# Kernel optimization log

Hardware: AMD Instinct MI355X
Metric: run time of the kernel (lower is better)

The kernel has to match this reference:

```python
import jax, jax.numpy as jnp
import numpy as np

# static config (levels=4, CDA=False branch -> self_attn_4, scale=4, f=False)
SHAPES = [(80, 80), (40, 40), (20, 20), (10, 10)]
D = 256; NH = 8; NL = 4; NP = 4; DFF = 1024; DH = D // NH
L = sum(h * w for h, w in SHAPES)  # 8500
B = 1


def layer_norm(x, g, b, eps=1e-5):
    m = jnp.mean(x, axis=-1, keepdims=True)
    v = jnp.mean((x - m) ** 2, axis=-1, keepdims=True)
    return (x - m) * jax.lax.rsqrt(v + eps) * g + b


def ms_deform_attn_core(value, loc, attn):
    # value: [B, L, NH, DH]; loc: [B, Lq, NH, NL, NP, 2] in [0,1]; attn: [B, Lq, NH, NL, NP]
    Bq, Lq = loc.shape[0], loc.shape[1]
    out = jnp.zeros((Bq, NH, Lq, DH), value.dtype)
    start = 0
    for lvl, (Hl, Wl) in enumerate(SHAPES):
        v = value[:, start:start + Hl * Wl]          # [B, HW, NH, DH]
        start += Hl * Wl
        v = v.transpose(0, 2, 1, 3)                  # [B, NH, HW, DH]
        ll = loc[:, :, :, lvl]                       # [B, Lq, NH, NP, 2]
        # grid_sample semantics: align_corners=False, padding_mode='zeros'
        x = ll[..., 0] * Wl - 0.5
        y = ll[..., 1] * Hl - 0.5
        x0 = jnp.floor(x); y0 = jnp.floor(y)
        acc = jnp.zeros((Bq, NH, Lq, NP, DH), value.dtype)
        for dy in (0, 1):
            for dx in (0, 1):
                xi = x0 + dx; yi = y0 + dy
                w = (1.0 - jnp.abs(x - xi)) * (1.0 - jnp.abs(y - yi))  # [B,Lq,NH,NP]
                valid = (xi >= 0) & (xi < Wl) & (yi >= 0) & (yi < Hl)
                xi_c = jnp.clip(xi, 0, Wl - 1).astype(jnp.int32)
                yi_c = jnp.clip(yi, 0, Hl - 1).astype(jnp.int32)
                lin = (yi_c * Wl + xi_c).transpose(0, 2, 1, 3).reshape(Bq, NH, Lq * NP)
                g = jnp.take_along_axis(v, lin[..., None], axis=2).reshape(Bq, NH, Lq, NP, DH)
                wv = (w * valid.astype(w.dtype)).transpose(0, 2, 1, 3)[..., None]
                acc = acc + g * wv
        aw = attn[:, :, :, lvl].transpose(0, 2, 1, 3)[..., None]  # [B,NH,Lq,NP,1]
        out = out + jnp.sum(acc * aw, axis=3)
    return out.transpose(0, 2, 1, 3).reshape(Bq, Lq, NH * DH)


def setup_inputs():
    key = jax.random.key(0)
    ks = jax.random.split(key, 24)
    s = 0.02
    d = {}
    d['src'] = jax.random.normal(ks[0], (B, L, D), jnp.float32)
    d['pos'] = jax.random.normal(ks[1], (B, L, D), jnp.float32)
    d['reference_points'] = jax.random.uniform(ks[2], (B, L, NL, 2), jnp.float32)
    d['spatial_shapes'] = jnp.array(SHAPES, jnp.int32)
    d['level_start_index'] = jnp.array(np.cumsum([0] + [h * w for h, w in SHAPES[:-1]]), jnp.int32)
    d['scale'] = 4
    # MSDeformAttn params
    d['Wo'] = jax.random.normal(ks[3], (D, NH * NL * NP * 2), jnp.float32) * s
    d['bo'] = jax.random.normal(ks[4], (NH * NL * NP * 2,), jnp.float32) * s
    d['Wa'] = jax.random.normal(ks[5], (D, NH * NL * NP), jnp.float32) * s
    d['ba'] = jax.random.normal(ks[6], (NH * NL * NP,), jnp.float32) * s
    d['Wv'] = jax.random.normal(ks[7], (D, D), jnp.float32) * s
    d['bv'] = jnp.zeros((D,), jnp.float32)
    d['Wout'] = jax.random.normal(ks[8], (D, D), jnp.float32) * s
    d['bout'] = jnp.zeros((D,), jnp.float32)
    # FFN + LayerNorms
    d['W1'] = jax.random.normal(ks[9], (D, DFF), jnp.float32) * s
    d['b1'] = jnp.zeros((DFF,), jnp.float32)
    d['W2'] = jax.random.normal(ks[10], (DFF, D), jnp.float32) * s
    d['b2'] = jnp.zeros((D,), jnp.float32)
    d['g1'] = jnp.ones((D,), jnp.float32); d['be1'] = jnp.zeros((D,), jnp.float32)
    d['g2'] = jnp.ones((D,), jnp.float32); d['be2'] = jnp.zeros((D,), jnp.float32)
    return d


def reference(src, pos, reference_points, spatial_shapes, level_start_index, scale,
              Wo, bo, Wa, ba, Wv, bv, Wout, bout, W1, b1, W2, b2, g1, be1, g2, be2):
    Bq, Lq, _ = src.shape
    q = src + pos  # with_pos_embed
    # sampling offsets & attention weights (softmax over levels*points)
    off = (q @ Wo + bo).reshape(Bq, Lq, NH, NL, NP, 2)
    attn = jax.nn.softmax((q @ Wa + ba).reshape(Bq, Lq, NH, NL * NP), axis=-1)
    attn = attn.reshape(Bq, Lq, NH, NL, NP)
    value = (src @ Wv + bv).reshape(Bq, L, NH, DH)
    # offset normalizer is (W, H) per level
    normalizer = jnp.stack([spatial_shapes[:, 1], spatial_shapes[:, 0]], -1).astype(src.dtype)
    loc = reference_points[:, :, None, :, None, :] + off / normalizer[None, None, None, :, None, :]
    src2 = ms_deform_attn_core(value, loc, attn) @ Wout + bout
    # residual + norm1 (dropout = eval identity)
    x = layer_norm(src + src2, g1, be1)
    # FFN
    ffn = jax.nn.relu(x @ W1 + b1) @ W2 + b2
    x = layer_norm(x + ffn, g2, be2)
    return x
```

## Files before the change

kernel.cpp:

```cpp
#include <hip/hip_runtime.h>
#include <hip/hip_bf16.h>
#include <string.h>

#define D 256
#define NH 8
#define DH 32
#define NL 4
#define NP 4
#define DFF 1024
#define LTOT 8500

typedef __bf16 bf16x8 __attribute__((ext_vector_type(8)));
typedef float floatx4 __attribute__((ext_vector_type(4)));

__device__ inline unsigned bpack(float a, float b) {
    __hip_bfloat16 ha = __float2bfloat16(a), hb = __float2bfloat16(b);
    unsigned short ua, ub;
    memcpy(&ua, &ha, 2); memcpy(&ub, &hb, 2);
    return (unsigned)ua | ((unsigned)ub << 16);
}

__device__ inline void gload16(const void* g, void* l) {
    __builtin_amdgcn_global_load_lds((const __attribute__((address_space(1))) void*)g,
                                     (__attribute__((address_space(3))) void*)l,
                                     16, 0, 0);
}

__global__ void transpose_all(const float* W0, const float* W1_, const float* W2_,
                              const float* W3, const float* W4, const float* W5,
                              __hip_bfloat16* T0, __hip_bfloat16* T1, __hip_bfloat16* T2,
                              __hip_bfloat16* T3, __hip_bfloat16* T4, __hip_bfloat16* T5,
                              const float* src, const float* pos,
                              __hip_bfloat16* qb, __hip_bfloat16* srcb) {
    int id = blockIdx.x;
    if (id >= 736) {
        int idx = (id - 736) * 2048 + threadIdx.x * 8;
        if (idx < LTOT * 256) {
            float4 s0 = *(const float4*)(src + idx);
            float4 s1 = *(const float4*)(src + idx + 4);
            float4 p0 = *(const float4*)(pos + idx);
            float4 p1 = *(const float4*)(pos + idx + 4);
            uint4 us, uq;
            us.x = bpack(s0.x, s0.y); us.y = bpack(s0.z, s0.w);
            us.z = bpack(s1.x, s1.y); us.w = bpack(s1.z, s1.w);
            uq.x = bpack(s0.x + p0.x, s0.y + p0.y); uq.y = bpack(s0.z + p0.z, s0.w + p0.w);
            uq.z = bpack(s1.x + p1.x, s1.y + p1.y); uq.w = bpack(s1.z + p1.z, s1.w + p1.w);
            *(uint4*)(srcb + idx) = us;
            *(uint4*)(qb + idx)  = uq;
        }
        return;
    }
    const int cum[7] = {0, 64, 96, 160, 224, 480, 736};
    int mi = 0;
    while (id >= cum[mi + 1]) mi++;
    int lid = id - cum[mi];
    const float* W; __hip_bfloat16* T; int K, N;
    switch (mi) {
        case 0: W = W0; T = T0; K = 256;  N = 256;  break;
        case 1: W = W1_; T = T1; K = 256; N = 128;  break;
        case 2: W = W2_; T = T2; K = 256; N = 256;  break;
        case 3: W = W3; T = T3; K = 256;  N = 256;  break;
        case 4: W = W4; T = T4; K = 256;  N = 1024; break;
        default: W = W5; T = T5; K = 1024; N = 256; break;
    }
    int ntx = N >> 5;
    int n0 = (lid % ntx) * 32, k0 = (lid / ntx) * 32;
    __shared__ float t[32][33];
    int tx = threadIdx.x & 31, ty = threadIdx.x >> 5;
#pragma unroll
    for (int i = 0; i < 32; i += 8)
        t[ty + i][tx] = W[(size_t)(k0 + ty + i) * N + n0 + tx];
    __syncthreads();
#pragma unroll
    for (int i = 0; i < 32; i += 8)
        T[(size_t)(n0 + ty + i) * K + k0 + tx] = __float2bfloat16(t[tx][ty + i]);
}

__global__ __launch_bounds__(256) void proj2(
    const __hip_bfloat16* __restrict__ qb, const __hip_bfloat16* __restrict__ srcb,
    const __hip_bfloat16* __restrict__ WoT, const __hip_bfloat16* __restrict__ WaT,
    const __hip_bfloat16* __restrict__ WvT,
    const float* __restrict__ bo, const float* __restrict__ ba, const float* __restrict__ bv,
    float* __restrict__ locb, float* __restrict__ attnb, __hip_bfloat16* __restrict__ valb,
    int M) {
    constexpr int BM = 64, BN = 64, BK = 64, K = 256;
    __shared__ __align__(16) __hip_bfloat16 sA[BM * BK];
    __shared__ __align__(16) __hip_bfloat16 sB[BN * BK];

    int n0 = blockIdx.x * BN;
    int m0 = blockIdx.y * BM;

    const __hip_bfloat16* BT;
    const __hip_bfloat16* A;
    const float* bias;
    int ncol0, Nout;
    float* Cf; __hip_bfloat16* Cb;
    if (n0 < 256)      { A = qb;   BT = WoT; bias = bo; ncol0 = n0;       Nout = 256; Cf = locb;  Cb = nullptr; }
    else if (n0 < 384) { A = qb;   BT = WaT; bias = ba; ncol0 = n0 - 256; Nout = 128; Cf = attnb; Cb = nullptr; }
    else               { A = srcb; BT = WvT; bias = bv; ncol0 = n0 - 384; Nout = 256; Cf = nullptr; Cb = valb; }

    int tid = threadIdx.x, wave = tid >> 6, lane = tid & 63;
    int wm = (wave >> 1) * 32, wn = (wave & 1) * 32;

    floatx4 acc[2][2];
#pragma unroll
    for (int i = 0; i < 2; i++)
#pragma unroll
        for (int j = 0; j < 2; j++)
#pragma unroll
            for (int e = 0; e < 4; e++) acc[i][j][e] = 0.f;

    int lrow = lane & 15, swz = lrow & 7;
    int scol = ((lane & 7) ^ (lane >> 3)) << 3;

    const __hip_bfloat16* aP[2];
    const __hip_bfloat16* bP[2];
#pragma unroll
    for (int i = 0; i < 2; i++) {
        int ra = m0 + i * 32 + wave * 8 + (lane >> 3); if (ra >= M) ra = M - 1;
        aP[i] = A + (size_t)ra * K + scol;
        int rb = ncol0 + i * 32 + wave * 8 + (lane >> 3);
        bP[i] = BT + (size_t)rb * K + scol;
    }
    int dOff = wave * 1024 + lane * 16;

    for (int k0 = 0; k0 < K; k0 += BK) {
#pragma unroll
        for (int i = 0; i < 2; i++) gload16(aP[i] + k0, (char*)sA + i * 4096 + dOff);
#pragma unroll
        for (int i = 0; i < 2; i++) gload16(bP[i] + k0, (char*)sB + i * 4096 + dOff);
        __syncthreads();
#pragma unroll
        for (int kk = 0; kk < 2; kk++) {
            int co = (((kk << 2) + (lane >> 4)) ^ swz) << 3;
            bf16x8 af[2], bfr[2];
#pragma unroll
            for (int tm = 0; tm < 2; tm++)
                af[tm] = *(const bf16x8*)(&sA[(wm + tm * 16 + lrow) * BK + co]);
#pragma unroll
            for (int tn = 0; tn < 2; tn++)
                bfr[tn] = *(const bf16x8*)(&sB[(wn + tn * 16 + lrow) * BK + co]);
#pragma unroll
            for (int tm = 0; tm < 2; tm++)
#pragma unroll
                for (int tn = 0; tn < 2; tn++)
                    acc[tm][tn] = __builtin_amdgcn_mfma_f32_16x16x32_bf16(af[tm], bfr[tn], acc[tm][tn], 0, 0, 0);
        }
        __syncthreads();
    }

    int lcol = lane & 15, lr4 = (lane >> 4) * 4;
#pragma unroll
    for (int tm = 0; tm < 2; tm++) {
#pragma unroll
        for (int i = 0; i < 4; i++) {
            int row = m0 + wm + tm * 16 + lr4 + i;
            if (row < M) {
#pragma unroll
                for (int tn = 0; tn < 2; tn++) {
                    int col = ncol0 + wn + tn * 16 + lcol;
                    float v = acc[tm][tn][i] + bias[col];
                    if (Cf) Cf[(size_t)row * Nout + col] = v;
                    else    Cb[(size_t)row * Nout + col] = __float2bfloat16(v);
                }
            }
        }
    }
}

__global__ __launch_bounds__(512) void deform_ln(
    const __hip_bfloat16* __restrict__ value,
    const float* __restrict__ locraw,
    const float* __restrict__ logits,
    const float* __restrict__ refp,
    const __hip_bfloat16* __restrict__ BT,
    const float* __restrict__ bias,
    const float* __restrict__ resid,
    const float* __restrict__ g, const float* __restrict__ be,
    float* __restrict__ outf, __hip_bfloat16* __restrict__ outb,
    int M) {
    __shared__ float wS[8][8][16][4];
    __shared__ int   aS[8][8][16][4];
    __shared__ __align__(16) __hip_bfloat16 aobL[16][264];
    __shared__ __align__(16) __hip_bfloat16 sB[256 * 64];
    __shared__ float psum[8][16], psq[8][16], mS[16], rS[16];

    int tid = threadIdx.x, wave = tid >> 6, lane = tid & 63;
    int m0 = blockIdx.x * 16;

    for (int r = 0; r < 2; r++) {
        int sub = tid >> 6, h = (tid >> 3) & 7, t8 = tid & 7;
        int q = m0 + r * 8 + sub; if (q >= M) q = M - 1;
        {
            const float* lg = logits + q * 128 + h * 16;
            float l0 = lg[t8], l1 = lg[t8 + 8];
            float mx = fmaxf(l0, l1);
#pragma unroll
            for (int m = 1; m < 8; m <<= 1) mx = fmaxf(mx, __shfl_xor(mx, m, 64));
            float e0 = __expf(l0 - mx), e1 = __expf(l1 - mx);
            float s = e0 + e1;
#pragma unroll
            for (int m = 1; m < 8; m <<= 1) s += __shfl_xor(s, m, 64);
            float inv = 1.f / s;

            const int starts[4] = {0, 6400, 8000, 8400};
#pragma unroll
            for (int j = 0; j < 2; j++) {
                int pp = t8 + 8 * j;
                float a = (j ? e1 : e0) * inv;
                int l = pp >> 2;
                int Wl = 80 >> l;
                float nv = (float)Wl;
                float rx = refp[q * 8 + l * 2 + 0];
                float ry = refp[q * 8 + l * 2 + 1];
                float lx = rx + locraw[q * 256 + h * 32 + pp * 2 + 0] / nv;
                float ly = ry + locraw[q * 256 + h * 32 + pp * 2 + 1] / nv;
                float x = lx * nv - 0.5f;
                float y = ly * nv - 0.5f;
                float x0f = floorf(x), y0f = floorf(y);
                float fx = x - x0f, fy = y - y0f;
                int x0 = (int)x0f, y0 = (int)y0f;
                float wts[4] = {(1.f - fx) * (1.f - fy), fx * (1.f - fy),
                                (1.f - fx) * fy,         fx * fy};
                int st = starts[l];
#pragma unroll
                for (int t = 0; t < 4; t++) {
                    int xi = x0 + (t & 1), yi = y0 + (t >> 1);
                    bool valid = (xi >= 0) & (xi < Wl) & (yi >= 0) & (yi < Wl);
                    int xc = min(max(xi, 0), Wl - 1), yc = min(max(yi, 0), Wl - 1);
                    wS[sub][h][pp][t] = valid ? wts[t] * a : 0.f;
                    aS[sub][h][pp][t] = (st + yc * Wl + xc) * 512 + h * 64;
                }
            }
        }
        __syncthreads();

        {
            int l8 = tid & 7;
            const char* vb = (const char*)value;
            int lo = l8 * 8;
            float a0 = 0.f, a1 = 0.f, a2 = 0.f, a3 = 0.f;
#pragma unroll
            for (int p = 0; p < 16; p++) {
                floatx4 w = *(const floatx4*)&wS[sub][h][p][0];
                int4 av = *(const int4*)&aS[sub][h][p][0];
#pragma unroll
                for (int t = 0; t < 4; t++) {
                    int ad = (t == 0) ? av.x : (t == 1) ? av.y : (t == 2) ? av.z : av.w;
                    uint2 u = *(const uint2*)(vb + ad + lo);
                    float wt = w[t];
                    a0 += wt * __uint_as_float(u.x << 16);
                    a1 += wt * __uint_as_float(u.x & 0xffff0000u);
                    a2 += wt * __uint_as_float(u.y << 16);
                    a3 += wt * __uint_as_float(u.y & 0xffff0000u);
                }
            }
            uint2 o;
            o.x = bpack(a0, a1);
            o.y = bpack(a2, a3);
            int lr = r * 8 + sub;
            *(uint2*)((char*)&aobL[0][0] + lr * 528 + h * 64 + l8 * 8) = o;
        }
        __syncthreads();
    }

    int lrow = lane & 15, swz = lrow & 7, q2 = lane >> 4;
    int scolB = ((tid & 7) ^ ((tid >> 3) & 7)) << 3;
    const __hip_bfloat16* bP[4];
#pragma unroll
    for (int i = 0; i < 4; i++)
        bP[i] = BT + (size_t)(i * 64 + (tid >> 3)) * 256 + scolB;

    floatx4 acc[2];
#pragma unroll
    for (int j = 0; j < 2; j++)
#pragma unroll
        for (int e = 0; e < 4; e++) acc[j][e] = 0.f;

    for (int t = 0; t < 4; t++) {
#pragma unroll
        for (int i = 0; i < 4; i++) gload16(bP[i] + t * 64, (char*)sB + i * 8192 + tid * 16);
        __syncthreads();
#pragma unroll
        for (int kk = 0; kk < 2; kk++) {
            int co = (((kk << 2) + q2) ^ swz) << 3;
            bf16x8 af = *(const bf16x8*)(&aobL[lrow][t * 64 + kk * 32 + q2 * 8]);
            bf16x8 bfr[2];
#pragma unroll
            for (int tn = 0; tn < 2; tn++)
                bfr[tn] = *(const bf16x8*)(&sB[(wave * 32 + tn * 16 + lrow) * 64 + co]);
#pragma unroll
            for (int tn = 0; tn < 2; tn++)
                acc[tn] = __builtin_amdgcn_mfma_f32_16x16x32_bf16(af, bfr[tn], acc[tn], 0, 0, 0);
        }
        __syncthreads();
    }

    int lcol = lane & 15, quad = lane >> 4;
    float v[2][4];
#pragma unroll
    for (int i = 0; i < 4; i++) {
        int row = quad * 4 + i;
        int grow = m0 + row; if (grow >= M) grow = M - 1;
#pragma unroll
        for (int tn = 0; tn < 2; tn++) {
            int col = wave * 32 + tn * 16 + lcol;
            v[tn][i] = acc[tn][i] + bias[col] + resid[(size_t)grow * 256 + col];
        }
    }

#pragma unroll
    for (int i = 0; i < 4; i++) {
        float s = 0.f, s2 = 0.f;
#pragma unroll
        for (int tn = 0; tn < 2; tn++) { float x = v[tn][i]; s += x; s2 += x * x; }
#pragma unroll
        for (int m = 1; m < 16; m <<= 1) {
            s  += __shfl_xor(s, m, 64);
            s2 += __shfl_xor(s2, m, 64);
        }
        if (lcol == 0) {
            int row = quad * 4 + i;
            psum[wave][row] = s;
            psq[wave][row]  = s2;
        }
    }
    __syncthreads();
    if (tid < 16) {
        float s = 0.f, s2 = 0.f;
#pragma unroll
        for (int w = 0; w < 8; w++) { s += psum[w][tid]; s2 += psq[w][tid]; }
        float m = s * (1.f / 256.f);
        float var = fmaxf(s2 * (1.f / 256.f) - m * m, 0.f);
        mS[tid] = m;
        rS[tid] = rsqrtf(var + 1e-5f);
    }
    __syncthreads();

#pragma unroll
    for (int i = 0; i < 4; i++) {
        int row = quad * 4 + i;
        int grow = m0 + row;
        if (grow < M) {
            float m = mS[row], rr = rS[row];
#pragma unroll
            for (int tn = 0; tn < 2; tn++) {
                int col = wave * 32 + tn * 16 + lcol;
                float o = (v[tn][i] - m) * rr * g[col] + be[col];
                outf[(size_t)grow * 256 + col] = o;
                outb[(size_t)grow * 256 + col] = __float2bfloat16(o);
            }
        }
    }
}

__global__ __launch_bounds__(512) void ffn(
    const __hip_bfloat16* __restrict__ A,
    const __hip_bfloat16* __restrict__ W1T,
    const float* __restrict__ b1,
    const __hip_bfloat16* __restrict__ W2T,
    const float* __restrict__ b2,
    const float* __restrict__ resid,
    const float* __restrict__ g, const float* __restrict__ be,
    float* __restrict__ outf, int M) {
    __shared__ __align__(16) __hip_bfloat16 sAx[16 * 256];
    __shared__ __align__(16) __hip_bfloat16 H[16 * 1032];
    __shared__ __align__(16) __hip_bfloat16 sB[256 * 64];
    __shared__ float psum[8][16], psq[8][16], mS[16], rS[16];

    int tid = threadIdx.x, wave = tid >> 6, lane = tid & 63;
    int m0 = blockIdx.x * 16;
    int lrow = lane & 15, swz = lrow & 7, q2 = lane >> 4;
    int quad = lane >> 4, lcol = lane & 15;
    int swzA = (lrow & 7) << 3;

    {
        int rr = tid >> 5, cc = tid & 31;
        int gr = m0 + rr; if (gr >= M) gr = M - 1;
        int colel = (cc * 8) ^ ((rr & 7) << 3);
        gload16(A + (size_t)gr * 256 + colel, (char*)sAx + tid * 16);
    }

    int scolB = ((tid & 7) ^ ((tid >> 3) & 7)) << 3;

    for (int c = 0; c < 4; c++) {
        const __hip_bfloat16* bP[4];
#pragma unroll
        for (int i = 0; i < 4; i++)
            bP[i] = W1T + (size_t)(c * 256 + i * 64 + (tid >> 3)) * 256 + scolB;

        floatx4 acc[2];
#pragma unroll
        for (int j = 0; j < 2; j++)
#pragma unroll
            for (int e = 0; e < 4; e++) acc[j][e] = 0.f;

        for (int t = 0; t < 4; t++) {
#pragma unroll
            for (int i = 0; i < 4; i++) gload16(bP[i] + t * 64, (char*)sB + i * 8192 + tid * 16);
            __syncthreads();
#pragma unroll
            for (int kk = 0; kk < 2; kk++) {
                int co = (((kk << 2) + q2) ^ swz) << 3;
                bf16x8 af = *(const bf16x8*)(&sAx[lrow * 256 + ((t * 64 + kk * 32 + q2 * 8) ^ swzA)]);
                bf16x8 bfr[2];
#pragma unroll
                for (int tn = 0; tn < 2; tn++)
                    bfr[tn] = *(const bf16x8*)(&sB[(wave * 32 + tn * 16 + lrow) * 64 + co]);
#pragma unroll
                for (int tn = 0; tn < 2; tn++)
                    acc[tn] = __builtin_amdgcn_mfma_f32_16x16x32_bf16(af, bfr[tn], acc[tn], 0, 0, 0);
            }
            __syncthreads();
        }

#pragma unroll
        for (int i = 0; i < 4; i++) {
            int row = quad * 4 + i;
#pragma unroll
            for (int tn = 0; tn < 2; tn++) {
                int col = c * 256 + wave * 32 + tn * 16 + lcol;
                float v = acc[tn][i] + b1[col];
                H[row * 1032 + col] = __float2bfloat16(fmaxf(v, 0.f));
            }
        }
    }

    const __hip_bfloat16* bP2[4];
#pragma unroll
    for (int i = 0; i < 4; i++)
        bP2[i] = W2T + (size_t)(i * 64 + (tid >> 3)) * 1024 + scolB;

    floatx4 acc2[2];
#pragma unroll
    for (int j = 0; j < 2; j++)
#pragma unroll
        for (int e = 0; e < 4; e++) acc2[j][e] = 0.f;

    for (int t = 0; t < 16; t++) {
#pragma unroll
        for (int i = 0; i < 4; i++) gload16(bP2[i] + t * 64, (char*)sB + i * 8192 + tid * 16);
        __syncthreads();
#pragma unroll
        for (int kk = 0; kk < 2; kk++) {
            int co = (((kk << 2) + q2) ^ swz) << 3;
            bf16x8 af = *(const bf16x8*)(&H[lrow * 1032 + t * 64 + kk * 32 + q2 * 8]);
            bf16x8 bfr[2];
#pragma unroll
            for (int tn = 0; tn < 2; tn++)
                bfr[tn] = *(const bf16x8*)(&sB[(wave * 32 + tn * 16 + lrow) * 64 + co]);
#pragma unroll
            for (int tn = 0; tn < 2; tn++)
                acc2[tn] = __builtin_amdgcn_mfma_f32_16x16x32_bf16(af, bfr[tn], acc2[tn], 0, 0, 0);
        }
        __syncthreads();
    }

    float v[2][4];
#pragma unroll
    for (int i = 0; i < 4; i++) {
        int row = quad * 4 + i;
        int grow = m0 + row; if (grow >= M) grow = M - 1;
#pragma unroll
        for (int tn = 0; tn < 2; tn++) {
            int col = wave * 32 + tn * 16 + lcol;
            v[tn][i] = acc2[tn][i] + b2[col] + resid[(size_t)grow * 256 + col];
        }
    }

#pragma unroll
    for (int i = 0; i < 4; i++) {
        float s = 0.f, s2 = 0.f;
#pragma unroll
        for (int tn = 0; tn < 2; tn++) { float x = v[tn][i]; s += x; s2 += x * x; }
#pragma unroll
        for (int m = 1; m < 16; m <<= 1) {
            s  += __shfl_xor(s, m, 64);
            s2 += __shfl_xor(s2, m, 64);
        }
        if (lcol == 0) {
            int row = quad * 4 + i;
            psum[wave][row] = s;
            psq[wave][row]  = s2;
        }
    }
    __syncthreads();
    if (tid < 16) {
        float s = 0.f, s2 = 0.f;
#pragma unroll
        for (int w = 0; w < 8; w++) { s += psum[w][tid]; s2 += psq[w][tid]; }
        float m = s * (1.f / 256.f);
        float var = fmaxf(s2 * (1.f / 256.f) - m * m, 0.f);
        mS[tid] = m;
        rS[tid] = rsqrtf(var + 1e-5f);
    }
    __syncthreads();

#pragma unroll
    for (int i = 0; i < 4; i++) {
        int row = quad * 4 + i;
        int grow = m0 + row;
        if (grow < M) {
            float m = mS[row], rr = rS[row];
#pragma unroll
            for (int tn = 0; tn < 2; tn++) {
                int col = wave * 32 + tn * 16 + lcol;
                outf[(size_t)grow * 256 + col] = (v[tn][i] - m) * rr * g[col] + be[col];
            }
        }
    }
}

extern "C" void kernel_launch(void* const* d_in, const int* in_sizes, int n_in,
                              void* d_out, int out_size, void* d_ws, size_t ws_size,
                              hipStream_t stream) {
    const float* src  = (const float*)d_in[0];
    const float* pos  = (const float*)d_in[1];
    const float* refp = (const float*)d_in[2];
    const float* Wo   = (const float*)d_in[6];
    const float* bo   = (const float*)d_in[7];
    const float* Wa   = (const float*)d_in[8];
    const float* ba   = (const float*)d_in[9];
    const float* Wv   = (const float*)d_in[10];
    const float* bv   = (const float*)d_in[11];
    const float* Wout = (const float*)d_in[12];
    const float* bout = (const float*)d_in[13];
    const float* W1   = (const float*)d_in[14];
    const float* b1   = (const float*)d_in[15];
    const float* W2   = (const float*)d_in[16];
    const float* b2   = (const float*)d_in[17];
    const float* g1   = (const float*)d_in[18];
    const float* be1  = (const float*)d_in[19];
    const float* g2   = (const float*)d_in[20];
    const float* be2  = (const float*)d_in[21];
    float* out = (float*)d_out;
    char* ws = (char*)d_ws;

    __hip_bfloat16* WoT   = (__hip_bfloat16*)(ws + 0);
    __hip_bfloat16* WaT   = (__hip_bfloat16*)(ws + 131072);
    __hip_bfloat16* WvT   = (__hip_bfloat16*)(ws + 196608);
    __hip_bfloat16* WoutT = (__hip_bfloat16*)(ws + 327680);
    __hip_bfloat16* W1T   = (__hip_bfloat16*)(ws + 458752);
    __hip_bfloat16* W2T   = (__hip_bfloat16*)(ws + 983040);
    float*          locb  = (float*)(ws + 1507328);
    float*          attnb = (float*)(ws + 10211328);
    __hip_bfloat16* valb  = (__hip_bfloat16*)(ws + 14563328);
    float*          x1    = (float*)(ws + 23267328);
    __hip_bfloat16* x1b   = (__hip_bfloat16*)(ws + 31971328);
    __hip_bfloat16* qb    = (__hip_bfloat16*)(ws + 36323328);
    __hip_bfloat16* srcb  = (__hip_bfloat16*)(ws + 36323328 + 4352000);

    transpose_all<<<736 + 1063, 256, 0, stream>>>(Wo, Wa, Wv, Wout, W1, W2,
                                                  WoT, WaT, WvT, WoutT, W1T, W2T,
                                                  src, pos, qb, srcb);

    proj2<<<dim3(10, 133), 256, 0, stream>>>(qb, srcb, WoT, WaT, WvT, bo, ba, bv,
                                             locb, attnb, valb, LTOT);

    deform_ln<<<532, 512, 0, stream>>>(valb, locb, attnb, refp, WoutT, bout,
                                       src, g1, be1, x1, x1b, LTOT);

    ffn<<<532, 512, 0, stream>>>(x1b, W1T, b1, W2T, b2, x1, g2, be2, out, LTOT);
}
```

Baseline: 218.1 us.

## Split deformable sampling into standalone kernel and fuse output projection into FFN

Deformable bilinear sampling now runs as its own small-block kernel (4 queries per 256-thread block, 2125 blocks) and writes bf16 aggregated features to the workspace. The Wout projection, first LayerNorm, FFN and second LayerNorm are fused into one tail kernel that keeps x1 in registers and shared memory, so the fp32 and bf16 x1 round-trips through global memory go away. The gather-heavy sampling gets more blocks and better latency hiding, and it no longer waits on the GEMM's large shared-memory tile. The cost is an extra bf16 buffer write and read, plus heavier register and shared-memory pressure in the fused tail kernel.

Measured after the change: 197.7 us (median of 2 runs). 9.4% less time.

```diff
diff --git a/kernel.cpp b/kernel.cpp
--- a/kernel.cpp
+++ b/kernel.cpp
@@ -168,200 +168,96 @@
     }
 }
 
-__global__ __launch_bounds__(512) void deform_ln(
-    const __hip_bfloat16* __restrict__ value,
-    const float* __restrict__ locraw,
-    const float* __restrict__ logits,
-    const float* __restrict__ refp,
-    const __hip_bfloat16* __restrict__ BT,
-    const float* __restrict__ bias,
-    const float* __restrict__ resid,
-    const float* __restrict__ g, const float* __restrict__ be,
-    float* __restrict__ outf, __hip_bfloat16* __restrict__ outb,
-    int M) {
-    __shared__ float wS[8][8][16][4];
-    __shared__ int   aS[8][8][16][4];
-    __shared__ __align__(16) __hip_bfloat16 aobL[16][264];
-    __shared__ __align__(16) __hip_bfloat16 sB[256 * 64];
-    __shared__ float psum[8][16], psq[8][16], mS[16], rS[16];
-
-    int tid = threadIdx.x, wave = tid >> 6, lane = tid & 63;
-    int m0 = blockIdx.x * 16;
-
-    for (int r = 0; r < 2; r++) {
+__global__ __launch_bounds__(256) void deform(const __hip_bfloat16* __restrict__ value,
+                                              const float* __restrict__ locraw,
+                                              const float* __restrict__ logits,
+                                              const float* __restrict__ refp,
+                                              __hip_bfloat16* __restrict__ out) {
+    __shared__ float wS[4][8][16][4];
+    __shared__ int   aS[4][8][16][4];
+    int tid = threadIdx.x;
+    int q0 = blockIdx.x * 4;
+
+    {
         int sub = tid >> 6, h = (tid >> 3) & 7, t8 = tid & 7;
-        int q = m0 + r * 8 + sub; if (q >= M) q = M - 1;
-        {
-            const float* lg = logits + q * 128 + h * 16;
-            float l0 = lg[t8], l1 = lg[t8 + 8];
-            float mx = fmaxf(l0, l1);
-#pragma unroll
-            for (int m = 1; m < 8; m <<= 1) mx = fmaxf(mx, __shfl_xor(mx, m, 64));
-            float e0 = __expf(l0 - mx), e1 = __expf(l1 - mx);
-            float s = e0 + e1;
-#pragma unroll
-            for (int m = 1; m < 8; m <<= 1) s += __shfl_xor(s, m, 64);
-            float inv = 1.f / s;
-
-            const int starts[4] = {0, 6400, 8000, 8400};
-#pragma unroll
-            for (int j = 0; j < 2; j++) {
-                int pp = t8 + 8 * j;
-                float a = (j ? e1 : e0) * inv;
-                int l = pp >> 2;
-                int Wl = 80 >> l;
-                float nv = (float)Wl;
-                float rx = refp[q * 8 + l * 2 + 0];
-                float ry = refp[q * 8 + l * 2 + 1];
-                float lx = rx + locraw[q * 256 + h * 32 + pp * 2 + 0] / nv;
-                float ly = ry + locraw[q * 256 + h * 32 + pp * 2 + 1] / nv;
-                float x = lx * nv - 0.5f;
-                float y = ly * nv - 0.5f;
-                float x0f = floorf(x), y0f = floorf(y);
-                float fx = x - x0f, fy = y - y0f;
-                int x0 = (int)x0f, y0 = (int)y0f;
-                float wts[4] = {(1.f - fx) * (1.f - fy), fx * (1.f - fy),
-                                (1.f - fx) * fy,         fx * fy};
-                int st = starts[l];
-#pragma unroll
-                for (int t = 0; t < 4; t++) {
-                    int xi = x0 + (t & 1), yi = y0 + (t >> 1);
-                    bool valid = (xi >= 0) & (xi < Wl) & (yi >= 0) & (yi < Wl);
-                    int xc = min(max(xi, 0), Wl - 1), yc = min(max(yi, 0), Wl - 1);
-                    wS[sub][h][pp][t] = valid ? wts[t] * a : 0.f;
-                    aS[sub][h][pp][t] = (st + yc * Wl + xc) * 512 + h * 64;
-                }
+        int q = q0 + sub;
+        const float* lg = logits + q * 128 + h * 16;
+        float l0 = lg[t8], l1 = lg[t8 + 8];
+        float mx = fmaxf(l0, l1);
+#pragma unroll
+        for (int m = 1; m < 8; m <<= 1) mx = fmaxf(mx, __shfl_xor(mx, m, 64));
+        float e0 = __expf(l0 - mx), e1 = __expf(l1 - mx);
+        float s = e0 + e1;
+#pragma unroll
+        for (int m = 1; m < 8; m <<= 1) s += __shfl_xor(s, m, 64);
+        float inv = 1.f / s;
+
+        const int starts[4] = {0, 6400, 8000, 8400};
+#pragma unroll
+        for (int j = 0; j < 2; j++) {
+            int pp = t8 + 8 * j;
+            float a = (j ? e1 : e0) * inv;
+            int l = pp >> 2;
+            int Wl = 80 >> l;
+            float nv = (float)Wl;
+            float rx = refp[q * 8 + l * 2 + 0];
+            float ry = refp[q * 8 + l * 2 + 1];
+            float lx = rx + locraw[q * 256 + h * 32 + pp * 2 + 0] / nv;
+            float ly = ry + locraw[q * 256 + h * 32 + pp * 2 + 1] / nv;
+            float x = lx * nv - 0.5f;
+            float y = ly * nv - 0.5f;
+            float x0f = floorf(x), y0f = floorf(y);
+            float fx = x - x0f, fy = y - y0f;
+            int x0 = (int)x0f, y0 = (int)y0f;
+            float wts[4] = {(1.f - fx) * (1.f - fy), fx * (1.f - fy),
+                            (1.f - fx) * fy,         fx * fy};
+            int st = starts[l];
+#pragma unroll
+            for (int t = 0; t < 4; t++) {
+                int xi = x0 + (t & 1), yi = y0 + (t >> 1);
+                bool valid = (xi >= 0) & (xi < Wl) & (yi >= 0) & (yi < Wl);
+                int xc = min(max(xi, 0), Wl - 1), yc = min(max(yi, 0), Wl - 1);
+                wS[sub][h][pp][t] = valid ? wts[t] * a : 0.f;
+                aS[sub][h][pp][t] = (st + yc * Wl + xc) * 512 + h * 64;
             }
         }
-        __syncthreads();
-
-        {
-            int l8 = tid & 7;
-            const char* vb = (const char*)value;
-            int lo = l8 * 8;
-            float a0 = 0.f, a1 = 0.f, a2 = 0.f, a3 = 0.f;
-#pragma unroll
-            for (int p = 0; p < 16; p++) {
-                floatx4 w = *(const floatx4*)&wS[sub][h][p][0];
-                int4 av = *(const int4*)&aS[sub][h][p][0];
-#pragma unroll
-                for (int t = 0; t < 4; t++) {
-                    int ad = (t == 0) ? av.x : (t == 1) ? av.y : (t == 2) ? av.z : av.w;
-                    uint2 u = *(const uint2*)(vb + ad + lo);
-                    float wt = w[t];
-                    a0 += wt * __uint_as_float(u.x << 16);
-                    a1 += wt * __uint_as_float(u.x & 0xffff0000u);
-                    a2 += wt * __uint_as_float(u.y << 16);
-                    a3 += wt * __uint_as_float(u.y & 0xffff0000u);
-                }
-            }
-            uint2 o;
-            o.x = bpack(a0, a1);
-            o.y = bpack(a2, a3);
-            int lr = r * 8 + sub;
-            *(uint2*)((char*)&aobL[0][0] + lr * 528 + h * 64 + l8 * 8) = o;
-        }
-        __syncthreads();
-    }
-
-    int lrow = lane & 15, swz = lrow & 7, q2 = lane >> 4;
-    int scolB = ((tid & 7) ^ ((tid >> 3) & 7)) << 3;
-    const __hip_bfloat16* bP[4];
-#pragma unroll
-    for (int i = 0; i < 4; i++)
-        bP[i] = BT + (size_t)(i * 64 + (tid >> 3)) * 256 + scolB;
-
-    floatx4 acc[2];
-#pragma unroll
-    for (int j = 0; j < 2; j++)
-#pragma unroll
-        for (int e = 0; e < 4; e++) acc[j][e] = 0.f;
-
-    for (int t = 0; t < 4; t++) {
-#pragma unroll
-        for (int i = 0; i < 4; i++) gload16(bP[i] + t * 64, (char*)sB + i * 8192 + tid * 16);
-        __syncthreads();
-#pragma unroll
-        for (int kk = 0; kk < 2; kk++) {
-            int co = (((kk << 2) + q2) ^ swz) << 3;
-            bf16x8 af = *(const bf16x8*)(&aobL[lrow][t * 64 + kk * 32 + q2 * 8]);
-            bf16x8 bfr[2];
-#pragma unroll
-            for (int tn = 0; tn < 2; tn++)
-                bfr[tn] = *(const bf16x8*)(&sB[(wave * 32 + tn * 16 + lrow) * 64 + co]);
-#pragma unroll
-            for (int tn = 0; tn < 2; tn++)
-                acc[tn] = __builtin_amdgcn_mfma_f32_16x16x32_bf16(af, bfr[tn], acc[tn], 0, 0, 0);
-        }
-        __syncthreads();
-    }
-
-    int lcol = lane & 15, quad = lane >> 4;
-    float v[2][4];
-#pragma unroll
-    for (int i = 0; i < 4; i++) {
-        int row = quad * 4 + i;
-        int grow = m0 + row; if (grow >= M) grow = M - 1;
-#pragma unroll
-        for (int tn = 0; tn < 2; tn++) {
-            int col = wave * 32 + tn * 16 + lcol;
-            v[tn][i] = acc[tn][i] + bias[col] + resid[(size_t)grow * 256 + col];
-        }
-    }
-
-#pragma unroll
-    for (int i = 0; i < 4; i++) {
-        float s = 0.f, s2 = 0.f;
-#pragma unroll
-        for (int tn = 0; tn < 2; tn++) { float x = v[tn][i]; s += x; s2 += x * x; }
-#pragma unroll
-        for (int m = 1; m < 16; m <<= 1) {
-            s  += __shfl_xor(s, m, 64);
-            s2 += __shfl_xor(s2, m, 64);
-        }
-        if (lcol == 0) {
-            int row = quad * 4 + i;
-            psum[wave][row] = s;
-            psq[wave][row]  = s2;
-        }
     }
     __syncthreads();
-    if (tid < 16) {
-        float s = 0.f, s2 = 0.f;
-#pragma unroll
-        for (int w = 0; w < 8; w++) { s += psum[w][tid]; s2 += psq[w][tid]; }
-        float m = s * (1.f / 256.f);
-        float var = fmaxf(s2 * (1.f / 256.f) - m * m, 0.f);
-        mS[tid] = m;
-        rS[tid] = rsqrtf(var + 1e-5f);
-    }
-    __syncthreads();
-
-#pragma unroll
-    for (int i = 0; i < 4; i++) {
-        int row = quad * 4 + i;
-        int grow = m0 + row;
-        if (grow < M) {
-            float m = mS[row], rr = rS[row];
-#pragma unroll
-            for (int tn = 0; tn < 2; tn++) {
-                int col = wave * 32 + tn * 16 + lcol;
-                float o = (v[tn][i] - m) * rr * g[col] + be[col];
-                outf[(size_t)grow * 256 + col] = o;
-                outb[(size_t)grow * 256 + col] = __float2bfloat16(o);
-            }
-        }
-    }
-}
-
-__global__ __launch_bounds__(512) void ffn(
-    const __hip_bfloat16* __restrict__ A,
-    const __hip_bfloat16* __restrict__ W1T,
-    const float* __restrict__ b1,
-    const __hip_bfloat16* __restrict__ W2T,
-    const float* __restrict__ b2,
-    const float* __restrict__ resid,
-    const float* __restrict__ g, const float* __restrict__ be,
+
+    int sub = tid >> 6, h = (tid >> 3) & 7, l8 = tid & 7;
+    int q = q0 + sub;
+    const char* vb = (const char*)value;
+    int lo = l8 * 8;
+    float a0 = 0.f, a1 = 0.f, a2 = 0.f, a3 = 0.f;
+#pragma unroll
+    for (int p = 0; p < 16; p++) {
+        floatx4 w = *(const floatx4*)&wS[sub][h][p][0];
+        int4 av = *(const int4*)&aS[sub][h][p][0];
+#pragma unroll
+        for (int t = 0; t < 4; t++) {
+            int ad = (t == 0) ? av.x : (t == 1) ? av.y : (t == 2) ? av.z : av.w;
+            uint2 u = *(const uint2*)(vb + ad + lo);
+            float wt = w[t];
+            a0 += wt * __uint_as_float(u.x << 16);
+            a1 += wt * __uint_as_float(u.x & 0xffff0000u);
+            a2 += wt * __uint_as_float(u.y << 16);
+            a3 += wt * __uint_as_float(u.y & 0xffff0000u);
+        }
+    }
+    uint2 o;
+    o.x = bpack(a0, a1);
+    o.y = bpack(a2, a3);
+    *(uint2*)((char*)out + q * 512 + h * 64 + l8 * 8) = o;
+}
+
+__global__ __launch_bounds__(512) void tail(
+    const __hip_bfloat16* __restrict__ aob,
+    const __hip_bfloat16* __restrict__ WoutT, const float* __restrict__ bout,
+    const float* __restrict__ src,
+    const float* __restrict__ g1, const float* __restrict__ be1,
+    const __hip_bfloat16* __restrict__ W1T, const float* __restrict__ b1,
+    const __hip_bfloat16* __restrict__ W2T, const float* __restrict__ b2,
+    const float* __restrict__ g2, const float* __restrict__ be2,
     float* __restrict__ outf, int M) {
     __shared__ __align__(16) __hip_bfloat16 sAx[16 * 256];
     __shared__ __align__(16) __hip_bfloat16 H[16 * 1032];
@@ -373,31 +269,108 @@
     int lrow = lane & 15, swz = lrow & 7, q2 = lane >> 4;
     int quad = lane >> 4, lcol = lane & 15;
     int swzA = (lrow & 7) << 3;
+    int scolB = ((tid & 7) ^ ((tid >> 3) & 7)) << 3;
 
     {
         int rr = tid >> 5, cc = tid & 31;
         int gr = m0 + rr; if (gr >= M) gr = M - 1;
         int colel = (cc * 8) ^ ((rr & 7) << 3);
-        gload16(A + (size_t)gr * 256 + colel, (char*)sAx + tid * 16);
-    }
-
-    int scolB = ((tid & 7) ^ ((tid >> 3) & 7)) << 3;
+        gload16(aob + (size_t)gr * 256 + colel, (char*)sAx + tid * 16);
+    }
+
+    const __hip_bfloat16* bP[4];
+#pragma unroll
+    for (int i = 0; i < 4; i++)
+        bP[i] = WoutT + (size_t)(i * 64 + (tid >> 3)) * 256 + scolB;
+
+    floatx4 acc[2];
+#pragma unroll
+    for (int j = 0; j < 2; j++)
+#pragma unroll
+        for (int e = 0; e < 4; e++) acc[j][e] = 0.f;
+
+    for (int t = 0; t < 4; t++) {
+#pragma unroll
+        for (int i = 0; i < 4; i++) gload16(bP[i] + t * 64, (char*)sB + i * 8192 + tid * 16);
+        __syncthreads();
+#pragma unroll
+        for (int kk = 0; kk < 2; kk++) {
+            int co = (((kk << 2) + q2) ^ swz) << 3;
+            bf16x8 af = *(const bf16x8*)(&sAx[lrow * 256 + ((t * 64 + kk * 32 + q2 * 8) ^ swzA)]);
+            bf16x8 bfr[2];
+#pragma unroll
+            for (int tn = 0; tn < 2; tn++)
+                bfr[tn] = *(const bf16x8*)(&sB[(wave * 32 + tn * 16 + lrow) * 64 + co]);
+#pragma unroll
+            for (int tn = 0; tn < 2; tn++)
+                acc[tn] = __builtin_amdgcn_mfma_f32_16x16x32_bf16(af, bfr[tn], acc[tn], 0, 0, 0);
+        }
+        __syncthreads();
+    }
+
+    float v1[2][4];
+#pragma unroll
+    for (int i = 0; i < 4; i++) {
+        int row = quad * 4 + i;
+        int grow = m0 + row; if (grow >= M) grow = M - 1;
+#pragma unroll
+        for (int tn = 0; tn < 2; tn++) {
+            int col = wave * 32 + tn * 16 + lcol;
+            v1[tn][i] = acc[tn][i] + bout[col] + src[(size_t)grow * 256 + col];
+        }
+    }
+#pragma unroll
+    for (int i = 0; i < 4; i++) {
+        float s = 0.f, s2 = 0.f;
+#pragma unroll
+        for (int tn = 0; tn < 2; tn++) { float x = v1[tn][i]; s += x; s2 += x * x; }
+#pragma unroll
+        for (int m = 1; m < 16; m <<= 1) {
+            s  += __shfl_xor(s, m, 64);
+            s2 += __shfl_xor(s2, m, 64);
+        }
+        if (lcol == 0) { int row = quad * 4 + i; psum[wave][row] = s; psq[wave][row] = s2; }
+    }
+    __syncthreads();
+    if (tid < 16) {
+        float s = 0.f, s2 = 0.f;
+#pragma unroll
+        for (int w = 0; w < 8; w++) { s += psum[w][tid]; s2 += psq[w][tid]; }
+        float m = s * (1.f / 256.f);
+        float var = fmaxf(s2 * (1.f / 256.f) - m * m, 0.f);
+        mS[tid] = m; rS[tid] = rsqrtf(var + 1e-5f);
+    }
+    __syncthreads();
+
+    float x1r[2][4];
+#pragma unroll
+    for (int i = 0; i < 4; i++) {
+        int row = quad * 4 + i;
+        float m = mS[row], r = rS[row];
+#pragma unroll
+        for (int tn = 0; tn < 2; tn++) {
+            int col = wave * 32 + tn * 16 + lcol;
+            float o = (v1[tn][i] - m) * r * g1[col] + be1[col];
+            x1r[tn][i] = o;
+            sAx[row * 256 + (col ^ ((row & 7) << 3))] = __float2bfloat16(o);
+        }
+    }
 
     for (int c = 0; c < 4; c++) {
-        const __hip_bfloat16* bP[4];
+        const __hip_bfloat16* bPc[4];
 #pragma unroll
         for (int i = 0; i < 4; i++)
-            bP[i] = W1T + (size_t)(c * 256 + i * 64 + (tid >> 3)) * 256 + scolB;
-
-        floatx4 acc[2];
+            bPc[i] = W1T + (size_t)(c * 256 + i * 64 + (tid >> 3)) * 256 + scolB;
+
+        floatx4 accA[2];
 #pragma unroll
         for (int j = 0; j < 2; j++)
 #pragma unroll
-            for (int e = 0; e < 4; e++) acc[j][e] = 0.f;
+            for (int e = 0; e < 4; e++) accA[j][e] = 0.f;
 
         for (int t = 0; t < 4; t++) {
 #pragma unroll
-            for (int i = 0; i < 4; i++) gload16(bP[i] + t * 64, (char*)sB + i * 8192 + tid * 16);
+            for (int i = 0; i < 4; i++) gload16(bPc[i] + t * 64, (char*)sB + i * 8192 + tid * 16);
             __syncthreads();
 #pragma unroll
             for (int kk = 0; kk < 2; kk++) {
@@ -409,7 +382,7 @@
                     bfr[tn] = *(const bf16x8*)(&sB[(wave * 32 + tn * 16 + lrow) * 64 + co]);
 #pragma unroll
                 for (int tn = 0; tn < 2; tn++)
-                    acc[tn] = __builtin_amdgcn_mfma_f32_16x16x32_bf16(af, bfr[tn], acc[tn], 0, 0, 0);
+                    accA[tn] = __builtin_amdgcn_mfma_f32_16x16x32_bf16(af, bfr[tn], accA[tn], 0, 0, 0);
             }
             __syncthreads();
         }
@@ -420,7 +393,7 @@
 #pragma unroll
             for (int tn = 0; tn < 2; tn++) {
                 int col = c * 256 + wave * 32 + tn * 16 + lcol;
-                float v = acc[tn][i] + b1[col];
+                float v = accA[tn][i] + b1[col];
                 H[row * 1032 + col] = __float2bfloat16(fmaxf(v, 0.f));
             }
         }
@@ -456,33 +429,26 @@
         __syncthreads();
     }
 
-    float v[2][4];
+    float v2[2][4];
 #pragma unroll
     for (int i = 0; i < 4; i++) {
-        int row = quad * 4 + i;
-        int grow = m0 + row; if (grow >= M) grow = M - 1;
 #pragma unroll
         for (int tn = 0; tn < 2; tn++) {
             int col = wave * 32 + tn * 16 + lcol;
-            v[tn][i] = acc2[tn][i] + b2[col] + resid[(size_t)grow * 256 + col];
-        }
-    }
-
+            v2[tn][i] = acc2[tn][i] + b2[col] + x1r[tn][i];
+        }
+    }
 #pragma unroll
     for (int i = 0; i < 4; i++) {
         float s = 0.f, s2 = 0.f;
 #pragma unroll
-        for (int tn = 0; tn < 2; tn++) { float x = v[tn][i]; s += x; s2 += x * x; }
+        for (int tn = 0; tn < 2; tn++) { float x = v2[tn][i]; s += x; s2 += x * x; }
 #pragma unroll
         for (int m = 1; m < 16; m <<= 1) {
             s  += __shfl_xor(s, m, 64);
             s2 += __shfl_xor(s2, m, 64);
         }
-        if (lcol == 0) {
-            int row = quad * 4 + i;
-            psum[wave][row] = s;
-            psq[wave][row]  = s2;
-        }
+        if (lcol == 0) { int row = quad * 4 + i; psum[wave][row] = s; psq[wave][row] = s2; }
     }
     __syncthreads();
     if (tid < 16) {
@@ -491,8 +457,7 @@
         for (int w = 0; w < 8; w++) { s += psum[w][tid]; s2 += psq[w][tid]; }
         float m = s * (1.f / 256.f);
         float var = fmaxf(s2 * (1.f / 256.f) - m * m, 0.f);
-        mS[tid] = m;
-        rS[tid] = rsqrtf(var + 1e-5f);
+        mS[tid] = m; rS[tid] = rsqrtf(var + 1e-5f);
     }
     __syncthreads();
 
@@ -501,11 +466,11 @@
         int row = quad * 4 + i;
         int grow = m0 + row;
         if (grow < M) {
-            float m = mS[row], rr = rS[row];
+            float m = mS[row], r = rS[row];
 #pragma unroll
             for (int tn = 0; tn < 2; tn++) {
                 int col = wave * 32 + tn * 16 + lcol;
-                outf[(size_t)grow * 256 + col] = (v[tn][i] - m) * rr * g[col] + be[col];
+                outf[(size_t)grow * 256 + col] = (v2[tn][i] - m) * r * g2[col] + be2[col];
             }
         }
     }
@@ -545,10 +510,9 @@
     float*          locb  = (float*)(ws + 1507328);
     float*          attnb = (float*)(ws + 10211328);
     __hip_bfloat16* valb  = (__hip_bfloat16*)(ws + 14563328);
-    float*          x1    = (float*)(ws + 23267328);
-    __hip_bfloat16* x1b   = (__hip_bfloat16*)(ws + 31971328);
-    __hip_bfloat16* qb    = (__hip_bfloat16*)(ws + 36323328);
-    __hip_bfloat16* srcb  = (__hip_bfloat16*)(ws + 36323328 + 4352000);
+    __hip_bfloat16* aob   = (__hip_bfloat16*)(ws + 18915328);
+    __hip_bfloat16* qb    = (__hip_bfloat16*)(ws + 23267328);
+    __hip_bfloat16* srcb  = (__hip_bfloat16*)(ws + 27619328);
 
     transpose_all<<<736 + 1063, 256, 0, stream>>>(Wo, Wa, Wv, Wout, W1, W2,
                                                   WoT, WaT, WvT, WoutT, W1T, W2T,
@@ -557,8 +521,8 @@
     proj2<<<dim3(10, 133), 256, 0, stream>>>(qb, srcb, WoT, WaT, WvT, bo, ba, bv,
                                              locb, attnb, valb, LTOT);
 
-    deform_ln<<<532, 512, 0, stream>>>(valb, locb, attnb, refp, WoutT, bout,
-                                       src, g1, be1, x1, x1b, LTOT);
-
-    ffn<<<532, 512, 0, stream>>>(x1b, W1T, b1, W2T, b2, x1, g2, be2, out, LTOT);
-}
+    deform<<<2125, 256, 0, stream>>>(valb, locb, attnb, refp, aob);
+
+    tail<<<532, 512, 0, stream>>>(aob, WoutT, bout, src, g1, be1,
+                                  W1T, b1, W2T, b2, g2, be2, out, LTOT);
+}
```
